# Kernel tuning notes

Measured on AMD Instinct MI355X. Metric: run time of the kernel, lower is better.

## Reference

```python
import jax, jax.numpy as jnp
import numpy as np


def setup_inputs() -> dict:
    key = jax.random.key(0)
    k1, k2, k3 = jax.random.split(key, 3)
    N, S, D = 8, 2048, 1024
    x = jax.random.normal(k1, (N, S, D), dtype=jnp.float32)
    # kaiming_normal_ on a (1,1,D) tensor: std = sqrt(2 / fan_in) with fan_in = D
    std = np.sqrt(2.0 / D).astype(np.float32)
    w_lhs = jax.random.normal(k2, (1, 1, D), dtype=jnp.float32) * std
    w_rhs = jax.random.normal(k3, (1, 1, D), dtype=jnp.float32) * std
    return {"x": x, "w_lhs": w_lhs, "w_rhs": w_rhs}


def reference(x, w_lhs, w_rhs):
    # x: (N, S, D); w_lhs/w_rhs: (1, 1, D) broadcast elementwise scales
    lhs = x * w_lhs                       # (N, S, D)
    rhs = x * w_rhs                       # (N, S, D)
    scores = jnp.einsum('nsd,ntd->nst', lhs, rhs)  # (N, S, S), no 1/sqrt(d) scaling
    attn = jax.nn.softmax(scores, axis=2)
    return jnp.einsum('nst,ntd->nsd', attn, x)     # (N, S, D)
```

## Files before the change

kernel.cpp:

```cpp
#include <hip/hip_runtime.h>
#include <hip/hip_bf16.h>
#include <stdint.h>

typedef unsigned short u16;
typedef unsigned int u32;
typedef __attribute__((ext_vector_type(8))) short bf16x8;
typedef __attribute__((ext_vector_type(4))) float f32x4;

#define S_DIM 2048
#define D_DIM 1024

__device__ __forceinline__ u16 f2bf(float f) {
  u32 u = __float_as_uint(f);
  u += 0x7FFFu + ((u >> 16) & 1u);
  return (u16)(u >> 16);
}

typedef const __attribute__((address_space(1))) u32* gas1p;
typedef __attribute__((address_space(3))) u32* las3p;

__device__ __forceinline__ void gload_lds16(const void* g, void* l) {
  __builtin_amdgcn_global_load_lds((gas1p)g, (las3p)l, 16, 0, 0);
}

__device__ __forceinline__ void mfma16(f32x4& c, bf16x8 a, bf16x8 b) {
  c = __builtin_amdgcn_mfma_f32_16x16x32_bf16(a, b, c, 0, 0, 0);
}

__global__ __launch_bounds__(256) void prep_kernel(
    const float* __restrict__ x, const float* __restrict__ wl,
    const float* __restrict__ wr, u16* __restrict__ Qb, u16* __restrict__ Kb,
    u16* __restrict__ Vt, float* __restrict__ lsum, int batch0) {
  const int S = S_DIM, D = D_DIM;
  int nz = blockIdx.z;
  const float* xb = x + (size_t)(batch0 + nz) * S * D;
  u16* Qn = Qb + (size_t)nz * S * D;
  u16* Kn = Kb + (size_t)nz * S * D;
  u16* Vn = Vt + (size_t)nz * D * S;
  int t0 = blockIdx.x * 64;
  int d0 = blockIdx.y * 64;
  int tid = threadIdx.x;
  int rl = tid >> 4;
  int cl = (tid & 15) << 2;

  if (blockIdx.y == 0 && tid < 64) lsum[(size_t)nz * S + t0 + tid] = 0.0f;

  __shared__ u16 ldsT[64][68];

  float4 a = *(const float4*)(wl + d0 + cl);
  float4 b = *(const float4*)(wr + d0 + cl);
  float wv0 = a.x * b.x, wv1 = a.y * b.y, wv2 = a.z * b.z, wv3 = a.w * b.w;

#pragma unroll
  for (int p = 0; p < 4; ++p) {
    int r = p * 16 + rl;
    float4 xv = *(const float4*)(xb + (size_t)(t0 + r) * D + d0 + cl);
    u16 q0 = f2bf(xv.x), q1 = f2bf(xv.y), q2 = f2bf(xv.z), q3 = f2bf(xv.w);
    u16 k0 = f2bf(xv.x * wv0), k1 = f2bf(xv.y * wv1);
    u16 k2 = f2bf(xv.z * wv2), k3 = f2bf(xv.w * wv3);
    uint2 qpk;
    qpk.x = (u32)q0 | ((u32)q1 << 16);
    qpk.y = (u32)q2 | ((u32)q3 << 16);
    *(uint2*)(Qn + (size_t)(t0 + r) * D + d0 + cl) = qpk;
    uint2 kpk;
    kpk.x = (u32)k0 | ((u32)k1 << 16);
    kpk.y = (u32)k2 | ((u32)k3 << 16);
    *(uint2*)(Kn + (size_t)(t0 + r) * D + d0 + cl) = kpk;
    ldsT[cl + 0][r] = q0;
    ldsT[cl + 1][r] = q1;
    ldsT[cl + 2][r] = q2;
    ldsT[cl + 3][r] = q3;
  }
  __syncthreads();
#pragma unroll
  for (int p = 0; p < 4; ++p) {
    int dr = p * 16 + rl;
    u16 v0 = ldsT[dr][cl + 0], v1 = ldsT[dr][cl + 1];
    u16 v2 = ldsT[dr][cl + 2], v3 = ldsT[dr][cl + 3];
    uint2 pk;
    pk.x = (u32)v0 | ((u32)v1 << 16);
    pk.y = (u32)v2 | ((u32)v3 << 16);
    *(uint2*)(Vn + (size_t)(d0 + dr) * S + t0 + cl) = pk;
  }
}

__device__ __forceinline__ void gemm_main(const u16* __restrict__ A,
                                          const u16* __restrict__ B, int m0,
                                          int n0, int ldk, int NT, char* cl,
                                          int tid, f32x4 (&acc)[8][4]) {
  int lane = tid & 63, w = tid >> 6;
  int lk = lane & 15, g8 = lane >> 4, l7 = lane & 7;
  int wr = w >> 2, wc = w & 3;
  int sA0 = (wr * 128 + lk) * 128;
  int sB0 = (wc * 64 + lk) * 128 + 32768;
  int sx0 = (g8 ^ l7) << 4;
  int sx1 = ((4 + g8) ^ l7) << 4;
  int r8 = lane >> 3;
  int kel = (l7 ^ r8) << 3;
  const u16* gAs = A + (size_t)(m0 + w * 16 + r8) * ldk + kel;
  const u16* gBs = B + (size_t)(n0 + w * 16 + r8) * ldk + kel;
  char* dA = cl + w * 2048;
  char* dB = cl + 32768 + w * 2048;

#define STG_ALL(kt_, b_)                                   \
  {                                                        \
    const u16* ga_ = gAs + (size_t)(kt_)*64;               \
    const u16* gb_ = gBs + (size_t)(kt_)*64;               \
    char* da_ = dA + (b_)*65536;                           \
    char* db_ = dB + (b_)*65536;                           \
    gload_lds16(ga_, da_);                                 \
    gload_lds16(ga_ + 8 * (size_t)ldk, da_ + 1024);        \
    gload_lds16(ga_ + 128 * (size_t)ldk, da_ + 16384);     \
    gload_lds16(ga_ + 136 * (size_t)ldk, da_ + 17408);     \
    gload_lds16(gb_, db_);                                 \
    gload_lds16(gb_ + 8 * (size_t)ldk, db_ + 1024);        \
    gload_lds16(gb_ + 128 * (size_t)ldk, db_ + 16384);     \
    gload_lds16(gb_ + 136 * (size_t)ldk, db_ + 17408);     \
  }

  STG_ALL(0, 0);
  asm volatile("s_waitcnt vmcnt(0)");
  __builtin_amdgcn_s_barrier();

#pragma unroll 1
  for (int kt = 0; kt < NT; ++kt) {
    int b = kt & 1;
    int bo = b * 65536;

    bf16x8 a0[8], a1[8], b0[4], b1[4];
#pragma unroll
    for (int m = 0; m < 8; ++m)
      a0[m] = *(const bf16x8*)(cl + bo + sA0 + m * 2048 + sx0);
#pragma unroll
    for (int n = 0; n < 4; ++n)
      b0[n] = *(const bf16x8*)(cl + bo + sB0 + n * 2048 + sx0);
    if (kt + 1 < NT) STG_ALL(kt + 1, b ^ 1);
#pragma unroll
    for (int m = 0; m < 8; ++m)
      a1[m] = *(const bf16x8*)(cl + bo + sA0 + m * 2048 + sx1);
#pragma unroll
    for (int n = 0; n < 4; ++n)
      b1[n] = *(const bf16x8*)(cl + bo + sB0 + n * 2048 + sx1);
    __builtin_amdgcn_sched_barrier(0);

    __builtin_amdgcn_s_setprio(1);
#pragma unroll
    for (int m = 0; m < 8; ++m)
#pragma unroll
      for (int n = 0; n < 4; ++n) mfma16(acc[m][n], a0[m], b0[n]);
#pragma unroll
    for (int m = 0; m < 8; ++m)
#pragma unroll
      for (int n = 0; n < 4; ++n) mfma16(acc[m][n], a1[m], b1[n]);
    __builtin_amdgcn_s_setprio(0);

    asm volatile("s_waitcnt vmcnt(0)");
    __builtin_amdgcn_s_barrier();
  }
#undef STG_ALL
}

__global__ __launch_bounds__(512, 2) void qk_exp_kernel(
    const u16* __restrict__ Qb, const u16* __restrict__ Kb,
    u16* __restrict__ P, float* __restrict__ lsum) {
  const int S = S_DIM, D = D_DIM;
  int gz = gridDim.z;
  int lid = blockIdx.x + (blockIdx.y << 3) + (blockIdx.z << 6);
  int cpx = gz << 3;
  int swz = (lid & 7) * cpx + (lid >> 3);
  int bx = swz & 7, by = (swz >> 3) & 7, bz = swz >> 6;

  const u16* A = Qb + (size_t)bz * S * D;
  const u16* B = Kb + (size_t)bz * S * D;
  u16* C = P + (size_t)bz * S * S;
  float* lrow = lsum + (size_t)bz * S;

  int m0 = bx * 256;
  int n0 = by * 256;
  int tid = threadIdx.x;

  __shared__ __align__(16) u16 lds[65536];
  f32x4 acc[8][4] = {};
  gemm_main(A, B, m0, n0, D, D / 64, (char*)lds, tid, acc);

  int lane = tid & 63, w = tid >> 6;
  int lk = lane & 15, g8 = lane >> 4;
  int wr = w >> 2, wc = w & 3;
  int rr = g8 << 2;
#pragma unroll
  for (int m = 0; m < 8; ++m) {
    int rowb = m0 + wr * 128 + m * 16 + rr;
    float rs[4] = {0.f, 0.f, 0.f, 0.f};
#pragma unroll
    for (int n = 0; n < 4; ++n) {
#pragma unroll
      for (int r = 0; r < 4; ++r) {
        float e = __expf(fminf(acc[m][n][r], 30.0f));
        rs[r] += e;
        C[(size_t)(rowb + r) * S + n0 + wc * 64 + n * 16 + lk] = f2bf(e);
      }
    }
#pragma unroll
    for (int d = 1; d < 16; d <<= 1) {
      rs[0] += __shfl_xor(rs[0], d);
      rs[1] += __shfl_xor(rs[1], d);
      rs[2] += __shfl_xor(rs[2], d);
      rs[3] += __shfl_xor(rs[3], d);
    }
    if (lk == 0) {
#pragma unroll
      for (int r = 0; r < 4; ++r) atomicAdd(&lrow[rowb + r], rs[r]);
    }
  }
}

__global__ __launch_bounds__(512, 2) void pv_kernel(
    const u16* __restrict__ P, const u16* __restrict__ Vt,
    const float* __restrict__ lsum, float* __restrict__ out) {
  const int S = S_DIM, D = D_DIM;
  int gz = gridDim.z;
  int lid = blockIdx.x + (blockIdx.y << 3) + (blockIdx.z << 5);
  int cpx = gz << 2;
  int swz = (lid & 7) * cpx + (lid >> 3);
  int bx = swz & 7, by = (swz >> 3) & 3, bz = swz >> 5;

  const u16* A = P + (size_t)bz * S * S;
  const u16* B = Vt + (size_t)bz * D * S;
  const float* lrow = lsum + (size_t)bz * S;
  float* Cn = out + (size_t)bz * S * D;

  int m0 = bx * 256;
  int n0 = by * 256;
  int tid = threadIdx.x;

  __shared__ __align__(16) u16 lds[65536];
  f32x4 acc[8][4] = {};
  gemm_main(A, B, m0, n0, S, S / 64, (char*)lds, tid, acc);

  int lane = tid & 63, w = tid >> 6;
  int lk = lane & 15, g8 = lane >> 4;
  int wr = w >> 2, wc = w & 3;
  int rr = g8 << 2;
#pragma unroll
  for (int m = 0; m < 8; ++m) {
    int rowb = m0 + wr * 128 + m * 16 + rr;
#pragma unroll
    for (int r = 0; r < 4; ++r) {
      float inv = __fdividef(1.0f, lrow[rowb + r]);
      float* cp = Cn + (size_t)(rowb + r) * D + n0 + wc * 64 + lk;
      cp[0] = acc[m][0][r] * inv;
      cp[16] = acc[m][1][r] * inv;
      cp[32] = acc[m][2][r] * inv;
      cp[48] = acc[m][3][r] * inv;
    }
  }
}

extern "C" void kernel_launch(void* const* d_in, const int* in_sizes, int n_in,
                              void* d_out, int out_size, void* d_ws,
                              size_t ws_size, hipStream_t stream) {
  const float* x = (const float*)d_in[0];
  const float* wl = (const float*)d_in[1];
  const float* wr = (const float*)d_in[2];
  float* out = (float*)d_out;
  const int N = 8, S = S_DIM, D = D_DIM;
  const size_t szQ = (size_t)S * D;
  const size_t szP = (size_t)S * S;

  int g = 8;
  while (g > 1) {
    size_t need = (size_t)g * (3 * szQ * 2 + szP * 2 + (size_t)S * 4);
    if (need <= ws_size) break;
    g >>= 1;
  }

  for (int b0 = 0; b0 < N; b0 += g) {
    u16* Qb = (u16*)d_ws;
    u16* Kb = Qb + (size_t)g * szQ;
    u16* Vt = Kb + (size_t)g * szQ;
    u16* Pp = Vt + (size_t)g * szQ;
    float* lsum = (float*)(Pp + (size_t)g * szP);
    hipLaunchKernelGGL(prep_kernel, dim3(S / 64, D / 64, g), dim3(256), 0,
                       stream, x, wl, wr, Qb, Kb, Vt, lsum, b0);
    hipLaunchKernelGGL(qk_exp_kernel, dim3(S / 256, S / 256, g), dim3(512), 0,
                       stream, Qb, Kb, Pp, lsum);
    hipLaunchKernelGGL(pv_kernel, dim3(S / 256, D / 256, g), dim3(512), 0,
                       stream, Pp, Vt, lsum, out + (size_t)b0 * S * D);
  }
}
```

Measured before the change: 255.7 us.

## Load B operand directly from global into registers, halve LDS staging

The B tile is no longer staged through LDS. Each wave loads its B fragments straight from global memory into registers every k-step, and only the A tile is double-buffered in LDS, which halves the shared memory footprint. This removes the LDS write/read traffic for B and could allow more blocks per CU. In exchange, the four waves sharing a column group redundantly load the same B data from global/L2, and those loads are not prefetched, so each MFMA phase waits on global latency.

```diff
diff --git a/kernel.cpp b/kernel.cpp
--- a/kernel.cpp
+++ b/kernel.cpp
@@ -92,72 +92,68 @@
   int lk = lane & 15, g8 = lane >> 4, l7 = lane & 7;
   int wr = w >> 2, wc = w & 3;
   int sA0 = (wr * 128 + lk) * 128;
-  int sB0 = (wc * 64 + lk) * 128 + 32768;
   int sx0 = (g8 ^ l7) << 4;
   int sx1 = ((4 + g8) ^ l7) << 4;
   int r8 = lane >> 3;
   int kel = (l7 ^ r8) << 3;
   const u16* gAs = A + (size_t)(m0 + w * 16 + r8) * ldk + kel;
-  const u16* gBs = B + (size_t)(n0 + w * 16 + r8) * ldk + kel;
+  const u16* gB0 = B + (size_t)(n0 + wc * 64 + lk) * ldk + g8 * 8;
   char* dA = cl + w * 2048;
-  char* dB = cl + 32768 + w * 2048;
-
-#define STG_ALL(kt_, b_)                                   \
-  {                                                        \
-    const u16* ga_ = gAs + (size_t)(kt_)*64;               \
-    const u16* gb_ = gBs + (size_t)(kt_)*64;               \
-    char* da_ = dA + (b_)*65536;                           \
-    char* db_ = dB + (b_)*65536;                           \
-    gload_lds16(ga_, da_);                                 \
-    gload_lds16(ga_ + 8 * (size_t)ldk, da_ + 1024);        \
-    gload_lds16(ga_ + 128 * (size_t)ldk, da_ + 16384);     \
-    gload_lds16(ga_ + 136 * (size_t)ldk, da_ + 17408);     \
-    gload_lds16(gb_, db_);                                 \
-    gload_lds16(gb_ + 8 * (size_t)ldk, db_ + 1024);        \
-    gload_lds16(gb_ + 128 * (size_t)ldk, db_ + 16384);     \
-    gload_lds16(gb_ + 136 * (size_t)ldk, db_ + 17408);     \
-  }
-
-  STG_ALL(0, 0);
+
+#define STG_A4(kt_, b_)                                  \
+  {                                                      \
+    const u16* g_ = gAs + (size_t)(kt_)*64;              \
+    char* d_ = dA + (b_)*32768;                          \
+    gload_lds16(g_, d_);                                 \
+    gload_lds16(g_ + 8 * (size_t)ldk, d_ + 1024);        \
+    gload_lds16(g_ + 128 * (size_t)ldk, d_ + 16384);     \
+    gload_lds16(g_ + 136 * (size_t)ldk, d_ + 17408);     \
+  }
+
+  STG_A4(0, 0);
   asm volatile("s_waitcnt vmcnt(0)");
   __builtin_amdgcn_s_barrier();
 
 #pragma unroll 1
   for (int kt = 0; kt < NT; ++kt) {
     int b = kt & 1;
-    int bo = b * 65536;
-
-    bf16x8 a0[8], a1[8], b0[4], b1[4];
+    int bo = b * 32768;
+
+    bf16x8 bv0[4], bv1[4];
+    const u16* gb = gB0 + (size_t)kt * 64;
+#pragma unroll
+    for (int nf = 0; nf < 4; ++nf)
+      bv0[nf] = *(const bf16x8*)(gb + (size_t)nf * 16 * ldk);
+#pragma unroll
+    for (int nf = 0; nf < 4; ++nf)
+      bv1[nf] = *(const bf16x8*)(gb + (size_t)nf * 16 * ldk + 32);
+
+    if (kt + 1 < NT) STG_A4(kt + 1, b ^ 1);
+
+    bf16x8 a0[8], a1[8];
 #pragma unroll
     for (int m = 0; m < 8; ++m)
       a0[m] = *(const bf16x8*)(cl + bo + sA0 + m * 2048 + sx0);
 #pragma unroll
-    for (int n = 0; n < 4; ++n)
-      b0[n] = *(const bf16x8*)(cl + bo + sB0 + n * 2048 + sx0);
-    if (kt + 1 < NT) STG_ALL(kt + 1, b ^ 1);
-#pragma unroll
     for (int m = 0; m < 8; ++m)
       a1[m] = *(const bf16x8*)(cl + bo + sA0 + m * 2048 + sx1);
-#pragma unroll
-    for (int n = 0; n < 4; ++n)
-      b1[n] = *(const bf16x8*)(cl + bo + sB0 + n * 2048 + sx1);
     __builtin_amdgcn_sched_barrier(0);
 
     __builtin_amdgcn_s_setprio(1);
 #pragma unroll
     for (int m = 0; m < 8; ++m)
 #pragma unroll
-      for (int n = 0; n < 4; ++n) mfma16(acc[m][n], a0[m], b0[n]);
-#pragma unroll
-    for (int m = 0; m < 8; ++m)
-#pragma unroll
-      for (int n = 0; n < 4; ++n) mfma16(acc[m][n], a1[m], b1[n]);
+      for (int n = 0; n < 4; ++n) mfma16(acc[m][n], a0[m], bv0[n]);
+#pragma unroll
+    for (int m = 0; m < 8; ++m)
+#pragma unroll
+      for (int n = 0; n < 4; ++n) mfma16(acc[m][n], a1[m], bv1[n]);
     __builtin_amdgcn_s_setprio(0);
 
     asm volatile("s_waitcnt vmcnt(0)");
     __builtin_amdgcn_s_barrier();
   }
-#undef STG_ALL
+#undef STG_A4
 }
 
 __global__ __launch_bounds__(512, 2) void qk_exp_kernel(
@@ -179,7 +175,7 @@
   int n0 = by * 256;
   int tid = threadIdx.x;
 
-  __shared__ __align__(16) u16 lds[65536];
+  __shared__ __align__(16) u16 lds[32768];
   f32x4 acc[8][4] = {};
   gemm_main(A, B, m0, n0, D, D / 64, (char*)lds, tid, acc);
 
@@ -233,7 +229,7 @@
   int n0 = by * 256;
   int tid = threadIdx.x;
 
-  __shared__ __align__(16) u16 lds[65536];
+  __shared__ __align__(16) u16 lds[32768];
   f32x4 acc[8][4] = {};
   gemm_main(A, B, m0, n0, S, S / 64, (char*)lds, tid, acc);
 
```

After: 336.6 us. +31.6%, slower.
